# Kernel tuning notes

Measured on AMD Instinct MI355X. Metric: run time of the kernel, lower is better.

Reference implementation:

```python
import jax, jax.numpy as jnp
import numpy as np

INF_H, INF_W = 384, 384   # infer_size (boxes are in this coordinate frame)
INP_H, INP_W = 768, 768   # input_size (network input resolution)
PH, PW = 7, 7             # output_size
MG = 4                    # max adaptive sampling grid (ceil(roi_dim/pooled) <= 4 for our boxes)
SPATIAL_SCALE = 1.0


def setup_inputs() -> dict:
    key = jax.random.key(0)
    k1, k2, k3, k4, k5 = jax.random.split(key, 5)
    B, C, Hf, Wf = 2, 64, 384, 384
    L = 512
    image_tensor = jax.random.normal(k1, (B, C, Hf, Wf), dtype=jnp.float32)
    # boxes in infer-size (384x384) coords, x2>x1, y2>y1, size in [4,28] px
    x1 = jax.random.uniform(k2, (B, L), minval=0.0, maxval=350.0)
    y1 = jax.random.uniform(k3, (B, L), minval=0.0, maxval=350.0)
    w = jax.random.uniform(k4, (B, L), minval=4.0, maxval=28.0)
    h = jax.random.uniform(k5, (B, L), minval=4.0, maxval=28.0)
    boxes = jnp.stack([x1, y1, x1 + w, y1 + h], axis=-1).astype(jnp.float32)
    return {"image_tensor": image_tensor, "boxes": boxes}


def _bilinear(feat, bidx, y, x):
    # feat: [B,C,H,W]; bidx: scalar int; y,x: [PH,MG,PW,MG]
    H, W = feat.shape[2], feat.shape[3]
    valid = (y > -1.0) & (y < H) & (x > -1.0) & (x < W)
    y = jnp.clip(y, 0.0, H - 1.0)
    x = jnp.clip(x, 0.0, W - 1.0)
    y0 = jnp.floor(y).astype(jnp.int32)
    x0 = jnp.floor(x).astype(jnp.int32)
    y1i = jnp.minimum(y0 + 1, H - 1)
    x1i = jnp.minimum(x0 + 1, W - 1)
    ly = y - y0
    lx = x - x0
    hy = 1.0 - ly
    hx = 1.0 - lx
    # advanced indexing -> [PH,MG,PW,MG,C] (channel last)
    v00 = feat[bidx, :, y0, x0]
    v01 = feat[bidx, :, y0, x1i]
    v10 = feat[bidx, :, y1i, x0]
    v11 = feat[bidx, :, y1i, x1i]
    val = ((hy * hx)[..., None] * v00 + (hy * lx)[..., None] * v01
           + (ly * hx)[..., None] * v10 + (ly * lx)[..., None] * v11)
    return jnp.where(valid[..., None], val, 0.0)


def _roi_align_one(feat, roi, bidx):
    # roi: [4] in feature-map coords; aligned=True -> -0.5 shift
    x1 = roi[0] * SPATIAL_SCALE - 0.5
    y1 = roi[1] * SPATIAL_SCALE - 0.5
    x2 = roi[2] * SPATIAL_SCALE - 0.5
    y2 = roi[3] * SPATIAL_SCALE - 0.5
    roi_w = x2 - x1
    roi_h = y2 - y1
    bin_w = roi_w / PW
    bin_h = roi_h / PH
    # adaptive sampling grid (sampling_ratio=-1): ceil(roi_dim/pooled_dim)
    gh = jnp.clip(jnp.ceil(roi_h / PH), 1.0, float(MG))
    gw = jnp.clip(jnp.ceil(roi_w / PW), 1.0, float(MG))
    ig = jnp.arange(MG, dtype=jnp.float32)
    ys = y1 + jnp.arange(PH, dtype=jnp.float32)[:, None] * bin_h + (ig[None, :] + 0.5) * bin_h / gh  # [PH,MG]
    xs = x1 + jnp.arange(PW, dtype=jnp.float32)[:, None] * bin_w + (ig[None, :] + 0.5) * bin_w / gw  # [PW,MG]
    Y = jnp.broadcast_to(ys[:, :, None, None], (PH, MG, PW, MG))
    X = jnp.broadcast_to(xs[None, None, :, :], (PH, MG, PW, MG))
    vals = _bilinear(feat, bidx, Y, X)  # [PH,MG,PW,MG,C]
    mask = ((ig < gh)[None, :, None, None] & (ig < gw)[None, None, None, :]).astype(vals.dtype)
    count = gh * gw
    pooled = jnp.sum(vals * mask[..., None], axis=(1, 3)) / count  # [PH,PW,C]
    return jnp.transpose(pooled, (2, 0, 1))  # [C,PH,PW]


def reference(image_tensor, boxes):
    B, C, Hf, Wf = image_tensor.shape
    L = boxes.shape[1]
    # module forward: rescale boxes from infer_size to input_size
    s1 = jnp.array([INP_W / INF_W, INP_H / INF_H, INP_W / INF_W, INP_H / INF_H], jnp.float32)
    # roi_align: rescale input coords to feature-map coords
    s2 = jnp.array([Wf / INP_W, Hf / INP_H, Wf / INP_W, Hf / INP_H], jnp.float32)
    rois = (boxes * s1 * s2).reshape(-1, 4)          # [B*L, 4]
    bidx = jnp.repeat(jnp.arange(B), L)              # [B*L]
    out = jax.vmap(lambda r, i: _roi_align_one(image_tensor, r, i))(rois, bidx)
    return out  # [B*L, C, PH, PW]
```

## Files before the change

### kernel.cpp

```cpp
#include <hip/hip_runtime.h>
#include <hip/hip_bf16.h>

#define HF 384
#define WF 384
#define PLANE (HF * WF)
#define PHH 7
#define PWW 7
#define NBIN 49
#define MG 4
#define CC 64
#define LL 512
#define BB 2

__device__ __forceinline__ unsigned short bf16_rne(float f) {
    unsigned int b = __float_as_uint(f);
    b += 0x7FFFu + ((b >> 16) & 1u);
    return (unsigned short)(b >> 16);
}
__device__ __forceinline__ float bf16lo(unsigned int u) {
    return __uint_as_float(u << 16);
}
__device__ __forceinline__ float bf16hi(unsigned int u) {
    return __uint_as_float(u & 0xffff0000u);
}

#define TPS 129
__global__ __launch_bounds__(256) void transpose_kernel(
    const float* __restrict__ img,
    unsigned short* __restrict__ imgT)
{
    __shared__ float tile[CC * TPS];
    const int b   = blockIdx.y;
    const int hw0 = blockIdx.x * 128;
    const int t   = threadIdx.x;

    const float* __restrict__ src = img + (size_t)b * CC * PLANE + hw0;
    const int c_sub = t >> 5;
    const int col   = (t & 31) * 4;
    #pragma unroll
    for (int i = 0; i < 8; ++i) {
        int c = i * 8 + c_sub;
        float4 v = *(const float4*)(src + (size_t)c * PLANE + col);
        tile[c * TPS + col + 0] = v.x;
        tile[c * TPS + col + 1] = v.y;
        tile[c * TPS + col + 2] = v.z;
        tile[c * TPS + col + 3] = v.w;
    }
    __syncthreads();

    uint2* __restrict__ dst = (uint2*)(imgT + ((size_t)b * PLANE + hw0) * CC);
    const int p = t & 15;
    #pragma unroll
    for (int i = 0; i < 8; ++i) {
        int hw = i * 16 + (t >> 4);
        float a0 = tile[(4 * p + 0) * TPS + hw];
        float a1 = tile[(4 * p + 1) * TPS + hw];
        float a2 = tile[(4 * p + 2) * TPS + hw];
        float a3 = tile[(4 * p + 3) * TPS + hw];
        unsigned int lo = (unsigned int)bf16_rne(a0) | ((unsigned int)bf16_rne(a1) << 16);
        unsigned int hi = (unsigned int)bf16_rne(a2) | ((unsigned int)bf16_rne(a3) << 16);
        dst[(size_t)hw * 16 + p] = make_uint2(lo, hi);
    }
}

__global__ __launch_bounds__(256) void gather_kernel(
    const unsigned short* __restrict__ imgT,
    const float* __restrict__ boxes,
    float* __restrict__ out)
{
    const int t    = threadIdx.x;
    const int wave = t >> 6;
    const int lane = t & 63;
    const int g    = blockIdx.x * 4 + wave;
    const int r    = g / 13;
    const int m    = g - r * 13;
    const int q    = lane >> 4;
    const int cq   = lane & 15;
    const int binr = m * 4 + q;
    const bool do_store = (binr < NBIN);
    const int bin  = do_store ? binr : (NBIN - 1);
    const int ph   = bin / PWW;
    const int pw   = bin - ph * PWW;
    const int b    = r >> 9;

    const float4 box = ((const float4*)boxes)[r];
    const float x1 = box.x - 0.5f, y1 = box.y - 0.5f;
    const float x2 = box.z - 0.5f, y2 = box.w - 0.5f;
    const float bin_w = (x2 - x1) * (1.0f / PWW);
    const float bin_h = (y2 - y1) * (1.0f / PHH);
    const float ghf = fminf(fmaxf(ceilf(bin_h), 1.0f), (float)MG);
    const float gwf = fminf(fmaxf(ceilf(bin_w), 1.0f), (float)MG);
    const int igh = (int)ghf, igw = (int)gwf;
    const float inv_count = 1.0f / (ghf * gwf);

    int   xo0[MG], xo1[MG];
    float lxw[MG], hxw[MG];
    const float bx = x1 + pw * bin_w;
    const float sw = bin_w / gwf;
    #pragma unroll
    for (int ix = 0; ix < MG; ++ix) {
        float x  = bx + (ix + 0.5f) * sw;
        float xc = fminf(fmaxf(x, 0.0f), (float)(WF - 1));
        int x0   = (int)floorf(xc);
        int x1i  = min(x0 + 1, WF - 1);
        float lx = xc - (float)x0;
        xo0[ix] = x0 * CC + 4 * cq;
        xo1[ix] = x1i * CC + 4 * cq;
        lxw[ix] = lx;
        hxw[ix] = 1.0f - lx;
    }

    const unsigned short* __restrict__ bp = imgT + (size_t)b * PLANE * CC;
    const float by = y1 + ph * bin_h;
    const float sh = bin_h / ghf;
    float acc0 = 0.f, acc1 = 0.f, acc2 = 0.f, acc3 = 0.f;
    #pragma unroll
    for (int iy = 0; iy < MG; ++iy) {
        if (iy < igh) {
            float y  = by + (iy + 0.5f) * sh;
            float yc = fminf(fmaxf(y, 0.0f), (float)(HF - 1));
            int y0   = (int)floorf(yc);
            int y1i  = min(y0 + 1, HF - 1);
            float ly = yc - (float)y0;
            float hy = 1.0f - ly;
            const int ro0 = y0 * (WF * CC);
            const int ro1 = y1i * (WF * CC);
            #pragma unroll
            for (int ix = 0; ix < MG; ++ix) {
                if (ix < igw) {
                    uint2 v00 = *(const uint2*)(bp + ro0 + xo0[ix]);
                    uint2 v01 = *(const uint2*)(bp + ro0 + xo1[ix]);
                    uint2 v10 = *(const uint2*)(bp + ro1 + xo0[ix]);
                    uint2 v11 = *(const uint2*)(bp + ro1 + xo1[ix]);
                    const float w00 = hy * hxw[ix], w01 = hy * lxw[ix];
                    const float w10 = ly * hxw[ix], w11 = ly * lxw[ix];
                    acc0 += w00 * bf16lo(v00.x) + w01 * bf16lo(v01.x)
                          + w10 * bf16lo(v10.x) + w11 * bf16lo(v11.x);
                    acc1 += w00 * bf16hi(v00.x) + w01 * bf16hi(v01.x)
                          + w10 * bf16hi(v10.x) + w11 * bf16hi(v11.x);
                    acc2 += w00 * bf16lo(v00.y) + w01 * bf16lo(v01.y)
                          + w10 * bf16lo(v10.y) + w11 * bf16lo(v11.y);
                    acc3 += w00 * bf16hi(v00.y) + w01 * bf16hi(v01.y)
                          + w10 * bf16hi(v10.y) + w11 * bf16hi(v11.y);
                }
            }
        }
    }
    if (do_store) {
        float* __restrict__ o = out + ((size_t)r * CC + 4 * cq) * NBIN + bin;
        o[0 * NBIN] = acc0 * inv_count;
        o[1 * NBIN] = acc1 * inv_count;
        o[2 * NBIN] = acc2 * inv_count;
        o[3 * NBIN] = acc3 * inv_count;
    }
}

#define CHB 8
#define WROWS 32
#define WCOLS 32
#define WSTRIDE 33
#define CH_STRIDE (WROWS * WSTRIDE)

__global__ __launch_bounds__(256) void roi_align_fallback(
    const float* __restrict__ img, const float* __restrict__ boxes,
    float* __restrict__ out)
{
    __shared__ float tile[CHB * CH_STRIDE];
    __shared__ float4 ytap[PHH * MG];
    __shared__ float4 xtap[PWW * MG];
    const int blk = blockIdx.x;
    const int r = blk >> 3, cg = blk & 7, b = r >> 9, tid = threadIdx.x;
    const float4 box = ((const float4*)boxes)[r];
    const float x1 = box.x - 0.5f, y1 = box.y - 0.5f;
    const float x2 = box.z - 0.5f, y2 = box.w - 0.5f;
    const float bin_w = (x2 - x1) * (1.0f / PWW);
    const float bin_h = (y2 - y1) * (1.0f / PHH);
    const float ghf = fminf(fmaxf(ceilf(bin_h), 1.0f), (float)MG);
    const float gwf = fminf(fmaxf(ceilf(bin_w), 1.0f), (float)MG);
    const int igh = (int)ghf, igw = (int)gwf;
    const float inv_count = 1.0f / (ghf * gwf);
    const int x_org = max(0, (int)floorf(x1));
    const int y_org = max(0, (int)floorf(y1));
    const int ye = min((int)floorf(fminf(fmaxf(y2, 0.f), (float)(HF - 1))) + 1, HF - 1);
    const int xe = min((int)floorf(fminf(fmaxf(x2, 0.f), (float)(WF - 1))) + 1, WF - 1);
    const int ry = min(WROWS, ye - y_org + 1);
    const int rx = min(WCOLS, xe - x_org + 1);
    if (tid < 56) {
        const bool isY = tid < 28;
        const int ti = isY ? tid : tid - 28;
        const int p = ti >> 2, ig = ti & 3;
        if (isY) {
            float y = y1 + p * bin_h + (ig + 0.5f) * (bin_h / ghf);
            float yc = fminf(fmaxf(y, 0.0f), (float)(HF - 1));
            int y0 = (int)floorf(yc); int y1i = min(y0 + 1, HF - 1);
            float ly = yc - (float)y0; float4 tv;
            tv.x = __int_as_float((y0 - y_org) * WSTRIDE);
            tv.y = __int_as_float((y1i - y_org) * WSTRIDE);
            tv.z = ly; tv.w = 1.0f - ly; ytap[ti] = tv;
        } else {
            float x = x1 + p * bin_w + (ig + 0.5f) * (bin_w / gwf);
            float xc = fminf(fmaxf(x, 0.0f), (float)(WF - 1));
            int x0 = (int)floorf(xc); int x1i = min(x0 + 1, WF - 1);
            float lx = xc - (float)x0; float4 tv;
            tv.x = __int_as_float(x0 - x_org);
            tv.y = __int_as_float(x1i - x_org);
            tv.z = lx; tv.w = 1.0f - lx; xtap[ti] = tv;
        }
    }
    const float* __restrict__ pbase = img + (size_t)(b * CC + cg * CHB) * PLANE;
    #pragma unroll 8
    for (int i = 0; i < CHB * WROWS * WCOLS / 256; ++i) {
        int li = i * 256 + tid;
        int ch = li >> 10, rem = li & 1023, row = rem >> 5, col = rem & 31;
        if (row < ry && col < rx)
            tile[ch * CH_STRIDE + row * WSTRIDE + col] =
                pbase[(size_t)ch * PLANE + (y_org + row) * WF + (x_org + col)];
    }
    __syncthreads();
    const size_t out_base = ((size_t)r * CC + cg * CHB) * NBIN;
    for (int o = tid; o < CHB * NBIN; o += 256) {
        const int c = o / NBIN, bin = o - c * NBIN;
        const int ph = bin / PWW, pw = bin - ph * PWW;
        const float* __restrict__ cb = tile + c * CH_STRIDE;
        float acc = 0.0f;
        #pragma unroll
        for (int iy = 0; iy < MG; ++iy) if (iy < igh) {
            float4 yt = ytap[ph * MG + iy];
            int ro0 = __float_as_int(yt.x), ro1 = __float_as_int(yt.y);
            float ly = yt.z, hy = yt.w;
            #pragma unroll
            for (int ix = 0; ix < MG; ++ix) if (ix < igw) {
                float4 xt = xtap[pw * MG + ix];
                int xi0 = __float_as_int(xt.x), xi1 = __float_as_int(xt.y);
                float lx = xt.z, hx = xt.w;
                acc += hy * (hx * cb[ro0 + xi0] + lx * cb[ro0 + xi1])
                     + ly * (hx * cb[ro1 + xi0] + lx * cb[ro1 + xi1]);
            }
        }
        out[out_base + o] = acc * inv_count;
    }
}

extern "C" void kernel_launch(void* const* d_in, const int* in_sizes, int n_in,
                              void* d_out, int out_size, void* d_ws, size_t ws_size,
                              hipStream_t stream) {
    const float* img   = (const float*)d_in[0];
    const float* boxes = (const float*)d_in[1];
    float* out = (float*)d_out;

    const size_t need = (size_t)BB * PLANE * CC * sizeof(unsigned short);
    if (ws_size >= need) {
        unsigned short* imgT = (unsigned short*)d_ws;
        dim3 tgrid(PLANE / 128, BB);
        transpose_kernel<<<tgrid, 256, 0, stream>>>(img, imgT);
        const int ggrid = (BB * LL * 13) / 4;
        gather_kernel<<<ggrid, 256, 0, stream>>>(imgT, boxes, out);
    } else {
        roi_align_fallback<<<BB * LL * 8, 256, 0, stream>>>(img, boxes, out);
    }
}
```

Before: 46.52 us.

## Stage each ROI's bf16 window in shared memory before bilinear gather

The gather kernel now assigns one block per ROI and channel half, cooperatively loads the ROI's up-to-30x30 pixel window (32 channels, bf16) into LDS, and precomputes the y/x sampling taps in shared arrays. Each of the 392 active threads then does its bilinear taps from LDS instead of from scattered global loads. This is meant to cut redundant global/L2 traffic, since neighbouring bins and samples reuse the same pixels. In exchange it adds a block-wide barrier, about 58KB of LDS per block which limits occupancy, and a full window load even for small boxes.

```diff
diff --git a/kernel.cpp b/kernel.cpp
--- a/kernel.cpp
+++ b/kernel.cpp
@@ -63,25 +63,21 @@
     }
 }
 
-__global__ __launch_bounds__(256) void gather_kernel(
+#define WROW 30
+#define TROW 901
+__global__ __launch_bounds__(512) void gather_kernel(
     const unsigned short* __restrict__ imgT,
     const float* __restrict__ boxes,
     float* __restrict__ out)
 {
-    const int t    = threadIdx.x;
-    const int wave = t >> 6;
-    const int lane = t & 63;
-    const int g    = blockIdx.x * 4 + wave;
-    const int r    = g / 13;
-    const int m    = g - r * 13;
-    const int q    = lane >> 4;
-    const int cq   = lane & 15;
-    const int binr = m * 4 + q;
-    const bool do_store = (binr < NBIN);
-    const int bin  = do_store ? binr : (NBIN - 1);
-    const int ph   = bin / PWW;
-    const int pw   = bin - ph * PWW;
-    const int b    = r >> 9;
+    __shared__ uint2  tile[8 * TROW];
+    __shared__ float4 ytap[PHH * MG];
+    __shared__ float4 xtap[PWW * MG];
+
+    const int r     = blockIdx.x >> 1;
+    const int chalf = blockIdx.x & 1;
+    const int b     = r >> 9;
+    const int t     = threadIdx.x;
 
     const float4 box = ((const float4*)boxes)[r];
     const float x1 = box.x - 0.5f, y1 = box.y - 0.5f;
@@ -93,61 +89,107 @@
     const int igh = (int)ghf, igw = (int)gwf;
     const float inv_count = 1.0f / (ghf * gwf);
 
-    int   xo0[MG], xo1[MG];
-    float lxw[MG], hxw[MG];
-    const float bx = x1 + pw * bin_w;
-    const float sw = bin_w / gwf;
-    #pragma unroll
-    for (int ix = 0; ix < MG; ++ix) {
-        float x  = bx + (ix + 0.5f) * sw;
-        float xc = fminf(fmaxf(x, 0.0f), (float)(WF - 1));
-        int x0   = (int)floorf(xc);
-        int x1i  = min(x0 + 1, WF - 1);
-        float lx = xc - (float)x0;
-        xo0[ix] = x0 * CC + 4 * cq;
-        xo1[ix] = x1i * CC + 4 * cq;
-        lxw[ix] = lx;
-        hxw[ix] = 1.0f - lx;
-    }
-
-    const unsigned short* __restrict__ bp = imgT + (size_t)b * PLANE * CC;
-    const float by = y1 + ph * bin_h;
-    const float sh = bin_h / ghf;
-    float acc0 = 0.f, acc1 = 0.f, acc2 = 0.f, acc3 = 0.f;
-    #pragma unroll
-    for (int iy = 0; iy < MG; ++iy) {
-        if (iy < igh) {
-            float y  = by + (iy + 0.5f) * sh;
+    const int x_org = max(0, (int)floorf(x1));
+    const int y_org = max(0, (int)floorf(y1));
+    const int xe = min((int)floorf(fminf(fmaxf(x2, 0.f), (float)(WF - 1))) + 1, WF - 1);
+    const int ye = min((int)floorf(fminf(fmaxf(y2, 0.f), (float)(HF - 1))) + 1, HF - 1);
+    const int rx = min(WROW, xe - x_org + 1);
+    const int ry = min(WROW, ye - y_org + 1);
+
+    if (t < 56) {
+        const bool isY = t < 28;
+        const int ti = isY ? t : t - 28;
+        const int p  = ti >> 2;
+        const int ig = ti & 3;
+        if (isY) {
+            float y  = y1 + p * bin_h + (ig + 0.5f) * (bin_h / ghf);
             float yc = fminf(fmaxf(y, 0.0f), (float)(HF - 1));
             int y0   = (int)floorf(yc);
             int y1i  = min(y0 + 1, HF - 1);
             float ly = yc - (float)y0;
-            float hy = 1.0f - ly;
-            const int ro0 = y0 * (WF * CC);
-            const int ro1 = y1i * (WF * CC);
-            #pragma unroll
-            for (int ix = 0; ix < MG; ++ix) {
-                if (ix < igw) {
-                    uint2 v00 = *(const uint2*)(bp + ro0 + xo0[ix]);
-                    uint2 v01 = *(const uint2*)(bp + ro0 + xo1[ix]);
-                    uint2 v10 = *(const uint2*)(bp + ro1 + xo0[ix]);
-                    uint2 v11 = *(const uint2*)(bp + ro1 + xo1[ix]);
-                    const float w00 = hy * hxw[ix], w01 = hy * lxw[ix];
-                    const float w10 = ly * hxw[ix], w11 = ly * lxw[ix];
-                    acc0 += w00 * bf16lo(v00.x) + w01 * bf16lo(v01.x)
-                          + w10 * bf16lo(v10.x) + w11 * bf16lo(v11.x);
-                    acc1 += w00 * bf16hi(v00.x) + w01 * bf16hi(v01.x)
-                          + w10 * bf16hi(v10.x) + w11 * bf16hi(v11.x);
-                    acc2 += w00 * bf16lo(v00.y) + w01 * bf16lo(v01.y)
-                          + w10 * bf16lo(v10.y) + w11 * bf16lo(v11.y);
-                    acc3 += w00 * bf16hi(v00.y) + w01 * bf16hi(v01.y)
-                          + w10 * bf16hi(v10.y) + w11 * bf16hi(v11.y);
+            float4 tv;
+            tv.x = __int_as_float((y0  - y_org) * WROW);
+            tv.y = __int_as_float((y1i - y_org) * WROW);
+            tv.z = ly; tv.w = 1.0f - ly;
+            ytap[ti] = tv;
+        } else {
+            float x  = x1 + p * bin_w + (ig + 0.5f) * (bin_w / gwf);
+            float xc = fminf(fmaxf(x, 0.0f), (float)(WF - 1));
+            int x0   = (int)floorf(xc);
+            int x1i  = min(x0 + 1, WF - 1);
+            float lx = xc - (float)x0;
+            float4 tv;
+            tv.x = __int_as_float(x0  - x_org);
+            tv.y = __int_as_float(x1i - x_org);
+            tv.z = lx; tv.w = 1.0f - lx;
+            xtap[ti] = tv;
+        }
+    }
+
+    const uint2* __restrict__ srcT =
+        (const uint2*)imgT + (size_t)b * PLANE * 16 + chalf * 8;
+    const int nidx = ry * (WROW * 8);
+    for (int idx = t; idx < nidx; idx += 512) {
+        const int yy  = idx / (WROW * 8);
+        const int rem = idx - yy * (WROW * 8);
+        const int xx  = rem >> 3;
+        const int cq  = rem & 7;
+        uint2 v = make_uint2(0u, 0u);
+        if (xx < rx)
+            v = srcT[((size_t)(y_org + yy) * WF + (x_org + xx)) * 16 + cq];
+        tile[cq * TROW + yy * WROW + xx] = v;
+    }
+    __syncthreads();
+
+    if (t < NBIN * 8) {
+        const int bin = t >> 3;
+        const int cq  = t & 7;
+        const int ph  = bin / PWW;
+        const int pw  = bin - ph * PWW;
+        const uint2* __restrict__ cb = tile + cq * TROW;
+
+        int   xo0[MG], xo1[MG];
+        float lxw[MG], hxw[MG];
+        #pragma unroll
+        for (int ix = 0; ix < MG; ++ix) {
+            float4 tv = xtap[pw * MG + ix];
+            xo0[ix] = __float_as_int(tv.x);
+            xo1[ix] = __float_as_int(tv.y);
+            lxw[ix] = tv.z;
+            hxw[ix] = tv.w;
+        }
+
+        float acc0 = 0.f, acc1 = 0.f, acc2 = 0.f, acc3 = 0.f;
+        #pragma unroll
+        for (int iy = 0; iy < MG; ++iy) {
+            if (iy < igh) {
+                float4 yt = ytap[ph * MG + iy];
+                const int ro0 = __float_as_int(yt.x);
+                const int ro1 = __float_as_int(yt.y);
+                const float ly = yt.z, hy = yt.w;
+                #pragma unroll
+                for (int ix = 0; ix < MG; ++ix) {
+                    if (ix < igw) {
+                        uint2 v00 = cb[ro0 + xo0[ix]];
+                        uint2 v01 = cb[ro0 + xo1[ix]];
+                        uint2 v10 = cb[ro1 + xo0[ix]];
+                        uint2 v11 = cb[ro1 + xo1[ix]];
+                        const float w00 = hy * hxw[ix], w01 = hy * lxw[ix];
+                        const float w10 = ly * hxw[ix], w11 = ly * lxw[ix];
+                        acc0 += w00 * bf16lo(v00.x) + w01 * bf16lo(v01.x)
+                              + w10 * bf16lo(v10.x) + w11 * bf16lo(v11.x);
+                        acc1 += w00 * bf16hi(v00.x) + w01 * bf16hi(v01.x)
+                              + w10 * bf16hi(v10.x) + w11 * bf16hi(v11.x);
+                        acc2 += w00 * bf16lo(v00.y) + w01 * bf16lo(v01.y)
+                              + w10 * bf16lo(v10.y) + w11 * bf16lo(v11.y);
+                        acc3 += w00 * bf16hi(v00.y) + w01 * bf16hi(v01.y)
+                              + w10 * bf16hi(v10.y) + w11 * bf16hi(v11.y);
+                    }
                 }
             }
         }
-    }
-    if (do_store) {
-        float* __restrict__ o = out + ((size_t)r * CC + 4 * cq) * NBIN + bin;
+        float* __restrict__ o =
+            out + ((size_t)r * CC + chalf * 32 + cq * 4) * NBIN + bin;
         o[0 * NBIN] = acc0 * inv_count;
         o[1 * NBIN] = acc1 * inv_count;
         o[2 * NBIN] = acc2 * inv_count;
@@ -253,8 +295,7 @@
         unsigned short* imgT = (unsigned short*)d_ws;
         dim3 tgrid(PLANE / 128, BB);
         transpose_kernel<<<tgrid, 256, 0, stream>>>(img, imgT);
-        const int ggrid = (BB * LL * 13) / 4;
-        gather_kernel<<<ggrid, 256, 0, stream>>>(imgT, boxes, out);
+        gather_kernel<<<BB * LL * 2, 512, 0, stream>>>(imgT, boxes, out);
     } else {
         roi_align_fallback<<<BB * LL * 8, 256, 0, stream>>>(img, boxes, out);
     }
```

Measured after the change: 52.96 us. +13.8%, slower.

## Sort ROIs spatially and swizzle gather blocks across XCDs for L2 locality

Applied to the files above, without the earlier changes.

Adds a single-block kernel that buckets ROIs by batch and a coarse 6x6 grid of box centers and computes a stable permutation by rank counting. The gather kernel reads ROIs through this permutation and remaps block indices so consecutive sorted ROIs land on the same XCD, improving L2 reuse of the transposed bf16 feature map. It costs an extra kernel launch and an indirect load per wave.

```diff
diff --git a/kernel.cpp b/kernel.cpp
--- a/kernel.cpp
+++ b/kernel.cpp
@@ -24,6 +24,33 @@
     return __uint_as_float(u & 0xffff0000u);
 }
 
+__global__ __launch_bounds__(1024) void sort_rois(
+    const float* __restrict__ boxes, int* __restrict__ perm)
+{
+    __shared__ unsigned char bk[1024];
+    const int t = threadIdx.x;
+    const float4 bx = ((const float4*)boxes)[t];
+    const float cx = 0.5f * (bx.x + bx.z);
+    const float cy = 0.5f * (bx.y + bx.w);
+    int bxi = min(5, max(0, (int)(cx * (1.0f / 64.0f))));
+    int byi = min(5, max(0, (int)(cy * (1.0f / 64.0f))));
+    const int key = (t >> 9) * 36 + byi * 6 + bxi;
+    bk[t] = (unsigned char)key;
+    __syncthreads();
+    int rank = 0;
+    const uchar4* bk4 = (const uchar4*)bk;
+    #pragma unroll 8
+    for (int i = 0; i < 256; ++i) {
+        uchar4 v = bk4[i];
+        const int i4 = i * 4;
+        rank += ((int)v.x < key) || ((int)v.x == key && (i4 + 0) < t);
+        rank += ((int)v.y < key) || ((int)v.y == key && (i4 + 1) < t);
+        rank += ((int)v.z < key) || ((int)v.z == key && (i4 + 2) < t);
+        rank += ((int)v.w < key) || ((int)v.w == key && (i4 + 3) < t);
+    }
+    perm[rank] = t;
+}
+
 #define TPS 129
 __global__ __launch_bounds__(256) void transpose_kernel(
     const float* __restrict__ img,
@@ -66,14 +93,17 @@
 __global__ __launch_bounds__(256) void gather_kernel(
     const unsigned short* __restrict__ imgT,
     const float* __restrict__ boxes,
+    const int* __restrict__ perm,
     float* __restrict__ out)
 {
     const int t    = threadIdx.x;
     const int wave = t >> 6;
     const int lane = t & 63;
-    const int g    = blockIdx.x * 4 + wave;
-    const int r    = g / 13;
-    const int m    = g - r * 13;
+    const int gblk = (blockIdx.x & 7) * 416 + (blockIdx.x >> 3);
+    const int g    = gblk * 4 + wave;
+    const int rs   = g / 13;
+    const int m    = g - rs * 13;
+    const int r    = perm[rs];
     const int q    = lane >> 4;
     const int cq   = lane & 15;
     const int binr = m * 4 + q;
@@ -248,13 +278,16 @@
     const float* boxes = (const float*)d_in[1];
     float* out = (float*)d_out;
 
-    const size_t need = (size_t)BB * PLANE * CC * sizeof(unsigned short);
+    const size_t imgT_bytes = (size_t)BB * PLANE * CC * sizeof(unsigned short);
+    const size_t need = imgT_bytes + 4096;
     if (ws_size >= need) {
         unsigned short* imgT = (unsigned short*)d_ws;
+        int* perm = (int*)((char*)d_ws + imgT_bytes);
+        sort_rois<<<1, 1024, 0, stream>>>(boxes, perm);
         dim3 tgrid(PLANE / 128, BB);
         transpose_kernel<<<tgrid, 256, 0, stream>>>(img, imgT);
         const int ggrid = (BB * LL * 13) / 4;
-        gather_kernel<<<ggrid, 256, 0, stream>>>(imgT, boxes, out);
+        gather_kernel<<<ggrid, 256, 0, stream>>>(imgT, boxes, perm, out);
     } else {
         roi_align_fallback<<<BB * LL * 8, 256, 0, stream>>>(img, boxes, out);
     }
```

New measurement: 87.43 us. 87.9% more time.
